# Kernel optimization log

Measured on AMD Instinct MI355X. Metric: run time of the kernel, lower is better.

Reference implementation:

```python
import jax, jax.numpy as jnp
import numpy as np

B, S, D_IN, D_OUT = 4, 2048, 1024, 1024


def setup_inputs() -> dict:
    key = jax.random.key(0)
    k1, k2, k3, k4 = jax.random.split(key, 4)
    scale = 1.0 / np.sqrt(D_IN)
    return {
        "x": jax.random.normal(k1, (B, S, D_IN), dtype=jnp.float32),
        # torch nn.Linear weights have shape [d_out, d_in]
        "Wq": jax.random.normal(k2, (D_OUT, D_IN), dtype=jnp.float32) * scale,
        "Wk": jax.random.normal(k3, (D_OUT, D_IN), dtype=jnp.float32) * scale,
        "Wv": jax.random.normal(k4, (D_OUT, D_IN), dtype=jnp.float32) * scale,
    }


def reference(x, Wq, Wk, Wv):
    # Linear projections (torch Linear: y = x @ W.T), no bias
    q = jnp.einsum('bsd,od->bso', x, Wq)
    k = jnp.einsum('bsd,od->bso', x, Wk)
    v = jnp.einsum('bsd,od->bso', x, Wv)
    s = q.shape[1]
    scores = jnp.einsum('bqd,bkd->bqk', q, k)  # [B, S, S]
    causal = jnp.tril(jnp.ones((s, s), dtype=bool))  # True = keep
    scores = jnp.where(causal[None], scores, -jnp.inf)
    scale = jnp.asarray(k.shape[-1], scores.dtype) ** 0.5
    weights = jax.nn.softmax(scores / scale, axis=-1)
    return jnp.einsum('bqk,bkd->bqd', weights, v)
```

## Files before the change

### kernel.cpp

```cpp
#include <hip/hip_runtime.h>

#define BATCH 4
#define SEQ   2048
#define DIM   1024
#define MTOT  (BATCH * SEQ)
#define BK    32

typedef __bf16 bf16x8 __attribute__((ext_vector_type(8)));
typedef __bf16 bf16x4 __attribute__((ext_vector_type(4)));
typedef float  f32x4  __attribute__((ext_vector_type(4)));

__device__ __forceinline__ void gl_lds16(const __bf16* g, __bf16* l) {
    __builtin_amdgcn_global_load_lds(
        (const __attribute__((address_space(1))) void*)g,
        (__attribute__((address_space(3))) void*)l,
        16, 0, 0);
}

__global__ __launch_bounds__(256) void cvt_all_kernel(
    const float* __restrict__ x,  const float* __restrict__ w0,
    const float* __restrict__ w1, const float* __restrict__ w2,
    __bf16* __restrict__ xd, __bf16* __restrict__ d0,
    __bf16* __restrict__ d1, __bf16* __restrict__ d2)
{
    const int bid = blockIdx.x;
    const float* s;
    __bf16* d;
    int base;
    if (bid < 4096)      { s = x;  d = xd; base = bid; }
    else if (bid < 4608) { s = w0; d = d0; base = bid - 4096; }
    else if (bid < 5120) { s = w1; d = d1; base = bid - 4608; }
    else                 { s = w2; d = d2; base = bid - 5120; }
    const int i = (base * 256 + threadIdx.x) * 8;
    const float4 a = *(const float4*)(s + i);
    const float4 b = *(const float4*)(s + i + 4);
    bf16x8 o;
    o[0] = (__bf16)a.x; o[1] = (__bf16)a.y; o[2] = (__bf16)a.z; o[3] = (__bf16)a.w;
    o[4] = (__bf16)b.x; o[5] = (__bf16)b.y; o[6] = (__bf16)b.z; o[7] = (__bf16)b.w;
    *(bf16x8*)(d + i) = o;
}

__device__ __forceinline__ void gemm_core(
    const __bf16* __restrict__ A, size_t lda,
    const __bf16* __restrict__ Bm, size_t ldb,
    int m0, int n0, int kTiles,
    __bf16* lA, __bf16* lB,
    f32x4 (&acc)[4][4])
{
    const int tid  = threadIdx.x;
    const int lane = tid & 63;
    const int wave = tid >> 6;
    const int wm = (wave >> 1) << 6;
    const int wn = (wave & 1) << 6;

#pragma unroll
    for (int i = 0; i < 4; ++i)
#pragma unroll
        for (int j = 0; j < 4; ++j)
            acc[i][j] = (f32x4){0.f, 0.f, 0.f, 0.f};

    for (int kt = 0; kt < kTiles; ++kt) {
        const int k0 = kt << 5;
        __syncthreads();
#pragma unroll
        for (int it = 0; it < 2; ++it) {
            const int f   = tid + (it << 8);
            const int row = f >> 2;
            const int col = (f & 3) << 3;
            gl_lds16(A  + (size_t)(m0 + row) * lda + (size_t)(k0 + col), lA + f * 8);
            gl_lds16(Bm + (size_t)(n0 + row) * ldb + (size_t)(k0 + col), lB + f * 8);
        }
        __syncthreads();

        bf16x8 af[4], bfr[4];
#pragma unroll
        for (int i = 0; i < 4; ++i) {
            af[i]  = *(const bf16x8*)(lA + (size_t)(wm + i * 16 + (lane & 15)) * BK + ((lane >> 4) << 3));
            bfr[i] = *(const bf16x8*)(lB + (size_t)(wn + i * 16 + (lane & 15)) * BK + ((lane >> 4) << 3));
        }
#pragma unroll
        for (int i = 0; i < 4; ++i)
#pragma unroll
            for (int j = 0; j < 4; ++j)
                acc[i][j] = __builtin_amdgcn_mfma_f32_16x16x32_bf16(af[i], bfr[j], acc[i][j], 0, 0, 0);
    }
}

__device__ __forceinline__ void store_tile_bf16(
    f32x4 (&acc)[4][4], __bf16* scratch, bool transpose, float scale,
    __bf16* dst, size_t ldo, size_t r0, size_t c0,
    bool expMask = false, bool diag = false)
{
    const int tid  = threadIdx.x;
    const int lane = tid & 63;
    const int wave = tid >> 6;
    const int wm = (wave >> 1) << 6, wn = (wave & 1) << 6;
    const int quad = lane >> 4;
    const int ln15 = lane & 15;

#pragma unroll
    for (int p = 0; p < 4; ++p) {
        __syncthreads();
        if (!transpose) {
            if (wm == ((p >> 1) << 6)) {
#pragma unroll
                for (int ih = 0; ih < 2; ++ih) {
                    const int i = ((p & 1) << 1) + ih;
                    const int lr = ih * 16 + quad * 4;
#pragma unroll
                    for (int j = 0; j < 4; ++j)
#pragma unroll
                        for (int r = 0; r < 4; ++r) {
                            const int lm = wm + ((p & 1) << 5) + lr + r;
                            const int ln = wn + j * 16 + ln15;
                            float v = acc[i][j][r] * scale;
                            if (expMask) {
                                v = (!diag || ln <= lm) ? __expf(v) : 0.f;
                            }
                            scratch[(lr + r) * 136 + wn + j * 16 + ln15] = (__bf16)v;
                        }
                }
            }
        } else {
            if (wn == ((p >> 1) << 6)) {
#pragma unroll
                for (int jh = 0; jh < 2; ++jh) {
                    const int j = ((p & 1) << 1) + jh;
                    const int lr = jh * 16 + ln15;
#pragma unroll
                    for (int i = 0; i < 4; ++i)
#pragma unroll
                        for (int r = 0; r < 4; ++r)
                            scratch[lr * 136 + wm + i * 16 + quad * 4 + r] =
                                (__bf16)(acc[i][j][r] * scale);
                }
            }
        }
        __syncthreads();
#pragma unroll
        for (int it = 0; it < 2; ++it) {
            const int g   = tid + (it << 8);
            const int row = g >> 4;
            const int col = (g & 15) << 3;
            *(bf16x8*)(dst + (r0 + p * 32 + row) * ldo + c0 + col) =
                *(const bf16x8*)(scratch + row * 136 + col);
        }
    }
}

__global__ __launch_bounds__(512, 2) void qkv_kernel(
    const __bf16* __restrict__ x,
    const __bf16* __restrict__ Wq,
    const __bf16* __restrict__ Wk,
    const __bf16* __restrict__ Wv,
    __bf16* __restrict__ Q, __bf16* __restrict__ Kb, __bf16* __restrict__ Vt)
{
    __shared__ __bf16 smem[65536];

    const int L  = blockIdx.x;
    const int g  = (L & 7) * 48 + (L >> 3);
    const int z  = g >> 7;
    const int rm = g & 127;
    const int m0 = (rm >> 2) << 8;
    const int n0 = (rm & 3) << 8;
    const __bf16* W = (z == 0) ? Wq : (z == 1) ? Wk : Wv;

    const int tid  = threadIdx.x;
    const int lane = tid & 63;
    const int ln15 = lane & 15;
    const int quad = lane >> 4;
    const int wave = tid >> 6;
    const int wm   = wave >> 2;
    const int wn   = wave & 3;

    const int r0  = tid >> 3;
    const int cst = ((tid & 7) << 3) ^ ((r0 & 4) ? 16 : 0);
    const __bf16* Ab = x + (size_t)m0 * DIM;
    const __bf16* Bb = W + (size_t)n0 * DIM;

    const int qx = (quad << 3) ^ ((ln15 & 4) ? 16 : 0);
    int aoff[4], boff[2];
#pragma unroll
    for (int i = 0; i < 4; ++i) aoff[i] = (wm * 64 + i * 16 + ln15) * 64 + qx;
#pragma unroll
    for (int j = 0; j < 2; ++j) boff[j] = (wn * 32 + j * 16 + ln15) * 64 + qx;

    f32x4 acc[8][4];
#pragma unroll
    for (int i = 0; i < 8; ++i)
#pragma unroll
        for (int j = 0; j < 4; ++j) acc[i][j] = (f32x4){0.f, 0.f, 0.f, 0.f};

#define STAGE_A(h, t) do {                                                    \
    const __bf16* gs_ = Ab + (size_t)((h) * 128 + r0) * DIM + ((t) << 6) + cst; \
    __bf16* ls_ = smem + (((t) & 1) * 32768 + (h) * 8192);                    \
    gl_lds16(gs_, ls_ + tid * 8);                                             \
    gl_lds16(gs_ + (size_t)64 * DIM, ls_ + tid * 8 + 4096); } while (0)
#define STAGE_B(h, t) do {                                                    \
    const __bf16* gs_ = Bb + (size_t)((h) * 128 + r0) * DIM + ((t) << 6) + cst; \
    __bf16* ls_ = smem + (((t) & 1) * 32768 + 16384 + (h) * 8192);            \
    gl_lds16(gs_, ls_ + tid * 8);                                             \
    gl_lds16(gs_ + (size_t)64 * DIM, ls_ + tid * 8 + 4096); } while (0)

    bf16x8 aF[4][2], bF[2][2];
#define LOAD_A(h) do { const __bf16* p_ = smem + cb_ * 32768 + (h) * 8192;    \
    _Pragma("unroll") for (int i_ = 0; i_ < 4; ++i_) {                        \
        aF[i_][0] = *(const bf16x8*)(p_ + aoff[i_]);                          \
        aF[i_][1] = *(const bf16x8*)(p_ + aoff[i_] + 32); } } while (0)
#define LOAD_B(h) do { const __bf16* p_ = smem + cb_ * 32768 + 16384 + (h) * 8192; \
    _Pragma("unroll") for (int j_ = 0; j_ < 2; ++j_) {                        \
        bF[j_][0] = *(const bf16x8*)(p_ + boff[j_]);                          \
        bF[j_][1] = *(const bf16x8*)(p_ + boff[j_] + 32); } } while (0)
#define MFMA_Q(mh, nh) do {                                                   \
    __builtin_amdgcn_s_setprio(1);                                            \
    _Pragma("unroll") for (int i_ = 0; i_ < 4; ++i_)                          \
    _Pragma("unroll") for (int j_ = 0; j_ < 2; ++j_) {                        \
        acc[(mh)*4+i_][(nh)*2+j_] = __builtin_amdgcn_mfma_f32_16x16x32_bf16(  \
            aF[i_][0], bF[j_][0], acc[(mh)*4+i_][(nh)*2+j_], 0, 0, 0);        \
        acc[(mh)*4+i_][(nh)*2+j_] = __builtin_amdgcn_mfma_f32_16x16x32_bf16(  \
            aF[i_][1], bF[j_][1], acc[(mh)*4+i_][(nh)*2+j_], 0, 0, 0); }      \
    __builtin_amdgcn_s_setprio(0); } while (0)

    const int nt = DIM / 64;

    STAGE_B(0, 0);
    STAGE_A(1, 0);
    STAGE_A(0, 0);
    STAGE_B(1, 0);
    STAGE_B(0, 1);
    STAGE_A(1, 1);
    asm volatile("s_waitcnt vmcnt(4)" ::: "memory");
    __builtin_amdgcn_s_barrier();

    for (int T = 0; T < nt; ++T) {
        const int cb_ = T & 1;
        LOAD_A(0); LOAD_B(0);
        if (T + 1 < nt) STAGE_A(0, T + 1);
        __builtin_amdgcn_s_barrier();
        MFMA_Q(0, 0);
        __builtin_amdgcn_s_barrier();
        LOAD_A(1);
        if (T + 1 < nt) STAGE_B(1, T + 1);
        __builtin_amdgcn_s_barrier();
        MFMA_Q(1, 0);
        __builtin_amdgcn_s_barrier();
        LOAD_B(1);
        if (T + 2 < nt) STAGE_B(0, T + 2);
        __builtin_amdgcn_s_barrier();
        MFMA_Q(1, 1);
        __builtin_amdgcn_s_barrier();
        LOAD_A(0);
        if (T + 2 < nt) {
            STAGE_A(1, T + 2);
            asm volatile("s_waitcnt vmcnt(4)" ::: "memory");
        } else if (T + 1 < nt) {
            asm volatile("s_waitcnt vmcnt(0)" ::: "memory");
        }
        __builtin_amdgcn_s_barrier();
        MFMA_Q(0, 1);
        __builtin_amdgcn_s_barrier();
    }
#undef STAGE_A
#undef STAGE_B
#undef LOAD_A
#undef LOAD_B
#undef MFMA_Q

    __syncthreads();
    __bf16* scratch = smem;

    if (z < 2) {
        __bf16* dst = (z == 0) ? Q : Kb;
#pragma unroll
        for (int h = 0; h < 2; ++h) {
#pragma unroll
            for (int im = 0; im < 4; ++im) {
                const int lr = wm * 64 + im * 16 + quad * 4;
#pragma unroll
                for (int nf = 0; nf < 4; ++nf) {
                    const int lc = (nf >> 1) * 128 + wn * 32 + (nf & 1) * 16 + ln15;
#pragma unroll
                    for (int r = 0; r < 4; ++r)
                        scratch[(lr + r) * 264 + lc] = (__bf16)acc[h * 4 + im][nf][r];
                }
            }
            __syncthreads();
#pragma unroll
            for (int it = 0; it < 8; ++it) {
                const int f = tid + (it << 9);
                const int row = f >> 5, blk = f & 31;
                *(bf16x8*)(dst + (size_t)(m0 + h * 128 + row) * DIM + n0 + blk * 8) =
                    *(const bf16x8*)(scratch + row * 264 + blk * 8);
            }
            __syncthreads();
        }
    } else {
        const size_t b  = (size_t)(m0 >> 11);
        const int  ms0  = m0 & (SEQ - 1);
        __bf16* dst = Vt + b * (size_t)DIM * SEQ;
#pragma unroll
        for (int h = 0; h < 2; ++h) {
#pragma unroll
            for (int jn = 0; jn < 2; ++jn) {
                const int lrow = wn * 32 + jn * 16 + ln15;
#pragma unroll
                for (int mf = 0; mf < 8; ++mf) {
                    const int lcol = (mf >> 2) * 128 + wm * 64 + (mf & 3) * 16 + quad * 4;
                    bf16x4 v;
#pragma unroll
                    for (int r = 0; r < 4; ++r) v[r] = (__bf16)acc[mf][h * 2 + jn][r];
                    *(bf16x4*)(scratch + lrow * 264 + lcol) = v;
                }
            }
            __syncthreads();
#pragma unroll
            for (int it = 0; it < 8; ++it) {
                const int f = tid + (it << 9);
                const int row = f >> 5, blk = f & 31;
                *(bf16x8*)(dst + (size_t)(n0 + h * 128 + row) * SEQ + ms0 + blk * 8) =
                    *(const bf16x8*)(scratch + row * 264 + blk * 8);
            }
            __syncthreads();
        }
    }
}

__global__ __launch_bounds__(256) void scores_kernel(
    const __bf16* __restrict__ Q, const __bf16* __restrict__ Kb,
    __bf16* __restrict__ Sc)
{
    const int L = blockIdx.x;
    const int g = (L & 7) * 68 + (L >> 3);
    const int b = g / 136;
    const int t = g - b * 136;
    int i = (int)((sqrtf(8.f * t + 1.f) - 1.f) * 0.5f);
    while ((i + 1) * (i + 2) / 2 <= t) ++i;
    while (i * (i + 1) / 2 > t) --i;
    const int j = t - i * (i + 1) / 2;

    __shared__ __bf16 smem[8192];
    __bf16* lA = smem;
    __bf16* lB = smem + 128 * BK;
    const __bf16* A  = Q  + (size_t)b * SEQ * DIM;
    const __bf16* Bm = Kb + (size_t)b * SEQ * DIM;

    f32x4 acc[4][4];
    gemm_core(A, DIM, Bm, DIM, i << 7, j << 7, DIM / BK, lA, lB, acc);

    store_tile_bf16(acc, smem, false, 0.03125f,
                    Sc + (size_t)b * SEQ * SEQ, SEQ,
                    (size_t)(i << 7), (size_t)(j << 7),
                    true, (i == j));
}

__global__ __launch_bounds__(256) void rowsum_kernel(
    const __bf16* __restrict__ Sc, float* __restrict__ invl)
{
    const int rg = blockIdx.x;
    const int b  = rg >> 11;
    const int r  = rg & (SEQ - 1);
    const __bf16* row = Sc + ((size_t)b * SEQ + r) * SEQ;

    const int tid  = threadIdx.x;
    const int lane = tid & 63;
    const int wv   = tid >> 6;
    const int width = ((r >> 7) + 1) << 7;
    const int c0 = tid << 3;

    float s = 0.f;
    if (c0 < width) {
        const bf16x8 in = *(const bf16x8*)(row + c0);
#pragma unroll
        for (int k = 0; k < 8; ++k) s += (float)in[k];
    }
#pragma unroll
    for (int off = 32; off > 0; off >>= 1)
        s += __shfl_xor(s, off);

    __shared__ float red[4];
    if (lane == 0) red[wv] = s;
    __syncthreads();
    if (tid == 0)
        invl[rg] = 1.f / (red[0] + red[1] + red[2] + red[3]);
}

__global__ __launch_bounds__(256) void pv_kernel(
    const __bf16* __restrict__ P, const __bf16* __restrict__ Vt,
    const float* __restrict__ invl, float* __restrict__ out)
{
    const int L = blockIdx.x;
    const int c = L & 7;
    const int k = L >> 3;
    const int b = c >> 1;
    const int i = 15 - (c & 1) - ((k >> 3) << 1);
    const int x = k & 7;

    __shared__ __bf16 smem[8192];
    __bf16* lA = smem;
    __bf16* lB = smem + 128 * BK;
    const __bf16* A  = P  + (size_t)b * SEQ * SEQ;
    const __bf16* Bm = Vt + (size_t)b * DIM * SEQ;

    f32x4 acc[4][4];
    gemm_core(A, SEQ, Bm, SEQ, i << 7, x << 7, (i + 1) * (128 / BK), lA, lB, acc);

    const int lane = threadIdx.x & 63;
    const int wave = threadIdx.x >> 6;
    const int wm = (wave >> 1) << 6, wn = (wave & 1) << 6;
#pragma unroll
    for (int ii = 0; ii < 4; ++ii)
#pragma unroll
        for (int jj = 0; jj < 4; ++jj)
#pragma unroll
            for (int r = 0; r < 4; ++r) {
                const int m = (i << 7) + wm + ii * 16 + ((lane >> 4) << 2) + r;
                const int n = (x << 7) + wn + jj * 16 + (lane & 15);
                out[((size_t)b * SEQ + m) * DIM + n] =
                    acc[ii][jj][r] * invl[(b << 11) + m];
            }
}

extern "C" void kernel_launch(void* const* d_in, const int* in_sizes, int n_in,
                              void* d_out, int out_size, void* d_ws, size_t ws_size,
                              hipStream_t stream) {
    const float* x  = (const float*)d_in[0];
    const float* Wq = (const float*)d_in[1];
    const float* Wk = (const float*)d_in[2];
    const float* Wv = (const float*)d_in[3];
    float* out = (float*)d_out;

    char* ws = (char*)d_ws;
    __bf16* Q  = (__bf16*)(ws);
    __bf16* Kb = (__bf16*)(ws + (16ull << 20));
    __bf16* Vt = (__bf16*)(ws + (32ull << 20));
    __bf16* Sc = (__bf16*)(ws + (48ull << 20));
    __bf16* Wqb = (__bf16*)(ws + (80ull << 20));
    __bf16* Wkb = (__bf16*)(ws + (82ull << 20));
    __bf16* Wvb = (__bf16*)(ws + (84ull << 20));
    float*  invl = (float*)(ws + (86ull << 20));
    __bf16* xb  = (__bf16*)d_out;

    cvt_all_kernel<<<dim3(5632), 256, 0, stream>>>(x, Wq, Wk, Wv, xb, Wqb, Wkb, Wvb);

    qkv_kernel    <<<dim3(384),  512, 0, stream>>>(xb, Wqb, Wkb, Wvb, Q, Kb, Vt);
    scores_kernel <<<dim3(544),  256, 0, stream>>>(Q, Kb, Sc);
    rowsum_kernel <<<dim3(MTOT), 256, 0, stream>>>(Sc, invl);
    pv_kernel     <<<dim3(512),  256, 0, stream>>>(Sc, Vt, invl, out);
}
```

Measured before the change: 243.9 us.

## Rotate LDS swizzle, reorder QKV GEMM staging, and one-wave-per-row rowsum

The QKV GEMM switches to a rotation-based LDS column swizzle in place of the XOR-16 pattern, aimed at removing bank conflicts on fragment reads. It also double-buffers B fragments and reorders the quadrant MFMA/stage schedule so that A fragments are reused across consecutive quadrants with fewer LDS reloads. The rowsum kernel now assigns one wave per row with a strided loop, which removes the LDS reduction and the block barrier and launches four times fewer blocks. The new schedule must keep staged tiles consistent with the changed waitcnt ordering, and the extra B fragment set raises register pressure.

Result: faster. 230.3 us (-5.6%).

```diff
diff --git a/kernel.cpp b/kernel.cpp
--- a/kernel.cpp
+++ b/kernel.cpp
@@ -174,16 +174,16 @@
     const int wn   = wave & 3;
 
     const int r0  = tid >> 3;
-    const int cst = ((tid & 7) << 3) ^ ((r0 & 4) ? 16 : 0);
+    const int cst = ((((tid & 7) + 8) - (r0 & 7)) & 7) << 3;
     const __bf16* Ab = x + (size_t)m0 * DIM;
     const __bf16* Bb = W + (size_t)n0 * DIM;
 
-    const int qx = (quad << 3) ^ ((ln15 & 4) ? 16 : 0);
+    const int cq = (((quad << 3) + ((ln15 & 7) << 3)) & 63);
     int aoff[4], boff[2];
 #pragma unroll
-    for (int i = 0; i < 4; ++i) aoff[i] = (wm * 64 + i * 16 + ln15) * 64 + qx;
-#pragma unroll
-    for (int j = 0; j < 2; ++j) boff[j] = (wn * 32 + j * 16 + ln15) * 64 + qx;
+    for (int i = 0; i < 4; ++i) aoff[i] = (wm * 64 + i * 16 + ln15) * 64 + cq;
+#pragma unroll
+    for (int j = 0; j < 2; ++j) boff[j] = (wn * 32 + j * 16 + ln15) * 64 + cq;
 
     f32x4 acc[8][4];
 #pragma unroll
@@ -202,62 +202,61 @@
     gl_lds16(gs_, ls_ + tid * 8);                                             \
     gl_lds16(gs_ + (size_t)64 * DIM, ls_ + tid * 8 + 4096); } while (0)
 
-    bf16x8 aF[4][2], bF[2][2];
+    bf16x8 aF[4][2], bF[2][2][2];
 #define LOAD_A(h) do { const __bf16* p_ = smem + cb_ * 32768 + (h) * 8192;    \
     _Pragma("unroll") for (int i_ = 0; i_ < 4; ++i_) {                        \
         aF[i_][0] = *(const bf16x8*)(p_ + aoff[i_]);                          \
-        aF[i_][1] = *(const bf16x8*)(p_ + aoff[i_] + 32); } } while (0)
-#define LOAD_B(h) do { const __bf16* p_ = smem + cb_ * 32768 + 16384 + (h) * 8192; \
+        aF[i_][1] = *(const bf16x8*)(p_ + (aoff[i_] ^ 32)); } } while (0)
+#define LOAD_B(s, h) do { const __bf16* p_ = smem + cb_ * 32768 + 16384 + (h) * 8192; \
     _Pragma("unroll") for (int j_ = 0; j_ < 2; ++j_) {                        \
-        bF[j_][0] = *(const bf16x8*)(p_ + boff[j_]);                          \
-        bF[j_][1] = *(const bf16x8*)(p_ + boff[j_] + 32); } } while (0)
-#define MFMA_Q(mh, nh) do {                                                   \
+        bF[s][j_][0] = *(const bf16x8*)(p_ + boff[j_]);                       \
+        bF[s][j_][1] = *(const bf16x8*)(p_ + (boff[j_] ^ 32)); } } while (0)
+#define MFMA_Q(mh, nh, s) do {                                                \
     __builtin_amdgcn_s_setprio(1);                                            \
     _Pragma("unroll") for (int i_ = 0; i_ < 4; ++i_)                          \
     _Pragma("unroll") for (int j_ = 0; j_ < 2; ++j_) {                        \
         acc[(mh)*4+i_][(nh)*2+j_] = __builtin_amdgcn_mfma_f32_16x16x32_bf16(  \
-            aF[i_][0], bF[j_][0], acc[(mh)*4+i_][(nh)*2+j_], 0, 0, 0);        \
+            aF[i_][0], bF[s][j_][0], acc[(mh)*4+i_][(nh)*2+j_], 0, 0, 0);     \
         acc[(mh)*4+i_][(nh)*2+j_] = __builtin_amdgcn_mfma_f32_16x16x32_bf16(  \
-            aF[i_][1], bF[j_][1], acc[(mh)*4+i_][(nh)*2+j_], 0, 0, 0); }      \
+            aF[i_][1], bF[s][j_][1], acc[(mh)*4+i_][(nh)*2+j_], 0, 0, 0); }   \
     __builtin_amdgcn_s_setprio(0); } while (0)
 
     const int nt = DIM / 64;
 
+    STAGE_A(0, 0);
     STAGE_B(0, 0);
+    STAGE_B(1, 0);
     STAGE_A(1, 0);
-    STAGE_A(0, 0);
-    STAGE_B(1, 0);
+    STAGE_A(0, 1);
     STAGE_B(0, 1);
-    STAGE_A(1, 1);
     asm volatile("s_waitcnt vmcnt(4)" ::: "memory");
     __builtin_amdgcn_s_barrier();
 
     for (int T = 0; T < nt; ++T) {
         const int cb_ = T & 1;
-        LOAD_A(0); LOAD_B(0);
-        if (T + 1 < nt) STAGE_A(0, T + 1);
-        __builtin_amdgcn_s_barrier();
-        MFMA_Q(0, 0);
+        LOAD_A(0); LOAD_B(0, 0);
+        if (T + 1 < nt) STAGE_B(1, T + 1);
+        __builtin_amdgcn_s_barrier();
+        MFMA_Q(0, 0, 0);
+        __builtin_amdgcn_s_barrier();
+        LOAD_B(1, 1);
+        if (T + 1 < nt) STAGE_A(1, T + 1);
+        __builtin_amdgcn_s_barrier();
+        MFMA_Q(0, 1, 1);
         __builtin_amdgcn_s_barrier();
         LOAD_A(1);
-        if (T + 1 < nt) STAGE_B(1, T + 1);
-        __builtin_amdgcn_s_barrier();
-        MFMA_Q(1, 0);
-        __builtin_amdgcn_s_barrier();
-        LOAD_B(1);
-        if (T + 2 < nt) STAGE_B(0, T + 2);
-        __builtin_amdgcn_s_barrier();
-        MFMA_Q(1, 1);
-        __builtin_amdgcn_s_barrier();
-        LOAD_A(0);
+        if (T + 2 < nt) STAGE_A(0, T + 2);
+        __builtin_amdgcn_s_barrier();
+        MFMA_Q(1, 1, 1);
+        __builtin_amdgcn_s_barrier();
         if (T + 2 < nt) {
-            STAGE_A(1, T + 2);
+            STAGE_B(0, T + 2);
             asm volatile("s_waitcnt vmcnt(4)" ::: "memory");
         } else if (T + 1 < nt) {
             asm volatile("s_waitcnt vmcnt(0)" ::: "memory");
         }
         __builtin_amdgcn_s_barrier();
-        MFMA_Q(0, 1);
+        MFMA_Q(1, 0, 0);
         __builtin_amdgcn_s_barrier();
     }
 #undef STAGE_A
@@ -356,19 +355,17 @@
 __global__ __launch_bounds__(256) void rowsum_kernel(
     const __bf16* __restrict__ Sc, float* __restrict__ invl)
 {
-    const int rg = blockIdx.x;
-    const int b  = rg >> 11;
-    const int r  = rg & (SEQ - 1);
-    const __bf16* row = Sc + ((size_t)b * SEQ + r) * SEQ;
-
     const int tid  = threadIdx.x;
     const int lane = tid & 63;
     const int wv   = tid >> 6;
+    const int rg   = blockIdx.x * 4 + wv;
+    const int b    = rg >> 11;
+    const int r    = rg & (SEQ - 1);
+    const __bf16* row = Sc + ((size_t)b * SEQ + r) * SEQ;
     const int width = ((r >> 7) + 1) << 7;
-    const int c0 = tid << 3;
 
     float s = 0.f;
-    if (c0 < width) {
+    for (int c0 = lane << 3; c0 < width; c0 += 512) {
         const bf16x8 in = *(const bf16x8*)(row + c0);
 #pragma unroll
         for (int k = 0; k < 8; ++k) s += (float)in[k];
@@ -376,12 +373,8 @@
 #pragma unroll
     for (int off = 32; off > 0; off >>= 1)
         s += __shfl_xor(s, off);
-
-    __shared__ float red[4];
-    if (lane == 0) red[wv] = s;
-    __syncthreads();
-    if (tid == 0)
-        invl[rg] = 1.f / (red[0] + red[1] + red[2] + red[3]);
+    if (lane == 0)
+        invl[rg] = 1.f / s;
 }
 
 __global__ __launch_bounds__(256) void pv_kernel(
@@ -444,6 +437,6 @@
 
     qkv_kernel    <<<dim3(384),  512, 0, stream>>>(xb, Wqb, Wkb, Wvb, Q, Kb, Vt);
     scores_kernel <<<dim3(544),  256, 0, stream>>>(Q, Kb, Sc);
-    rowsum_kernel <<<dim3(MTOT), 256, 0, stream>>>(Sc, invl);
+    rowsum_kernel <<<dim3(2048), 256, 0, stream>>>(Sc, invl);
     pv_kernel     <<<dim3(512),  256, 0, stream>>>(Sc, Vt, invl, out);
 }
```
